# Performance work log

Measured on AMD Instinct MI355X. Metric: run time of the kernel, lower is better.

## Reference

```python
import jax, jax.numpy as jnp
import numpy as np

PENALTY_LAMBDA = 0.5
MAX_RULES = 512
INIT_GATE_LOGIT = -2.0


def setup_inputs() -> dict:
    key = jax.random.key(0)
    k1, k2, k3 = jax.random.split(key, 3)
    B, V, E = 64, 128000, 1000000
    logits = jax.random.normal(k1, (B, V), dtype=jnp.float32)
    # learned per-rule gate logits (nn.Parameter initialized at init_gate_logit;
    # we perturb slightly so gradients are non-degenerate)
    gate_logits = jnp.full((MAX_RULES,), INIT_GATE_LOGIT, dtype=jnp.float32) \
        + 0.1 * jax.random.normal(k2, (MAX_RULES,), dtype=jnp.float32)
    # flattened ragged (rule, token) violation pairs
    kr, kt = jax.random.split(k3)
    rule_ids = jax.random.randint(kr, (E,), 0, MAX_RULES, dtype=jnp.int32)
    token_ids = jax.random.randint(kt, (E,), 0, V, dtype=jnp.int32)
    return {"logits": logits, "gate_logits": gate_logits,
            "rule_ids": rule_ids, "token_ids": token_ids}


def reference(logits, gate_logits, rule_ids, token_ids):
    # eval-mode binary concrete gate (no noise, no thresholding): sigmoid(logit)
    gates = jax.nn.sigmoid(gate_logits)                      # [R]
    V = logits.shape[-1]
    # gated penalty value per (rule, token) pair, single vectorized scatter-add
    vals = gates[rule_ids] * jnp.asarray(PENALTY_LAMBDA, logits.dtype)  # [E]
    pen_1d = jnp.zeros((V,), dtype=logits.dtype).at[token_ids].add(vals)  # [V]
    penalties = jnp.broadcast_to(pen_1d[None, :], logits.shape)           # [B,V]
    modified = logits - penalties
    # coverage loss: -mean of gates over rules that fire (have >=1 violation)
    firing = jnp.zeros((MAX_RULES,), dtype=logits.dtype).at[rule_ids].set(1.0)
    n_firing = jnp.maximum(firing.sum(), 1.0)
    coverage_loss = -(gates * firing).sum() / n_firing
    return modified, coverage_loss, penalties
```

## Files before the change

kernel.cpp:

```cpp
#include <hip/hip_runtime.h>

#define PENALTY_LAMBDA 0.5f
#define RULES 512
#define NR 4
#define RS 32000
#define VOCAB 128000
#define G 64
#define NB 64
#define CH 500
#define CJ 125

typedef float    f32x4 __attribute__((ext_vector_type(4)));
typedef _Float16 f16x4 __attribute__((ext_vector_type(4)));


__global__ void __launch_bounds__(1024) scatter_kernel(
    const int* __restrict__ rule_ids, const int* __restrict__ token_ids,
    const float* __restrict__ gate_logits, _Float16* __restrict__ partials,
    unsigned* __restrict__ masks, int E) {
    __shared__ __align__(16) float hist[RS];
    __shared__ float s_g[RULES];
    __shared__ unsigned char s_f[RULES];
    int t = threadIdx.x;
    int g = blockIdx.x;
    int r = blockIdx.y;
    for (int i = t * 4; i < RS; i += 1024 * 4)
        *(f32x4*)(hist + i) = (f32x4){0.f, 0.f, 0.f, 0.f};
    if (t < RULES) {
        float x = gate_logits[t];
        s_g[t] = PENALTY_LAMBDA / (1.0f + expf(-x));
    }
    if (t >= 512 && t < 512 + RULES / 4) ((unsigned*)s_f)[t - 512] = 0u;
    __syncthreads();

    const int lo = r * RS;
    const int stride = G * 1024 * 4;
    for (int base = (g * 1024 + t) * 4; base + 4 <= E; base += stride) {
        int4 tt = *(const int4*)(token_ids + base);
        int4 rr = *(const int4*)(rule_ids + base);
        int ts[4] = {tt.x, tt.y, tt.z, tt.w};
        int rv[4] = {rr.x, rr.y, rr.z, rr.w};
#pragma unroll
        for (int k = 0; k < 4; ++k) {
            int tok = ts[k] - lo;
            if ((unsigned)tok < (unsigned)RS) atomicAdd(&hist[tok], s_g[rv[k]]);
            if (r == 0) s_f[rv[k]] = 1;
        }
    }
    if (g == 0 && t == 0) {
        for (int e = E & ~3; e < E; ++e) {
            int tok = token_ids[e] - lo; int ru = rule_ids[e];
            if ((unsigned)tok < (unsigned)RS) atomicAdd(&hist[tok], s_g[ru]);
            if (r == 0) s_f[ru] = 1;
        }
    }
    __syncthreads();

    _Float16* dst = partials + ((size_t)r * G + g) * RS;
    for (int i = t * 4; i < RS; i += 1024 * 4) {
        f32x4 s = *(const f32x4*)(&hist[i]);
        f16x4 h = {(_Float16)s.x, (_Float16)s.y, (_Float16)s.z, (_Float16)s.w};
        *(f16x4*)(dst + i) = h;
    }

    if (r == 0 && t < 16) {
        const unsigned* w = (const unsigned*)s_f + t * 8;
        unsigned m = 0;
#pragma unroll
        for (int k = 0; k < 8; ++k) {
            unsigned d = w[k];
            if (d & 0x000000FFu) m |= 1u << (k * 4 + 0);
            if (d & 0x0000FF00u) m |= 1u << (k * 4 + 1);
            if (d & 0x00FF0000u) m |= 1u << (k * 4 + 2);
            if (d & 0xFF000000u) m |= 1u << (k * 4 + 3);
        }
        masks[g * 16 + t] = m;
    }
}

__global__ void __launch_bounds__(512) fused_kernel(
    const _Float16* __restrict__ partials, const unsigned* __restrict__ masks,
    const float* __restrict__ gate_logits, const float* __restrict__ logits,
    float* __restrict__ out_mod, float* __restrict__ out_pen,
    float* __restrict__ out_loss) {
    __shared__ float s_pc[CH + 4];
    __shared__ f32x4 s_part[4][CJ + 1];
    int t = threadIdx.x;
    int tx = t & 127, ty = t >> 7;
    int chunk = blockIdx.x;
    int c0 = chunk * CH;
    int r = c0 / RS;
    int bin = c0 - r * RS;

    {
        if (tx < CJ) {
            f32x4 acc = {0.f, 0.f, 0.f, 0.f};
            const _Float16* bp = partials + ((size_t)r * G + ty * 16) * RS
                               + bin + tx * 4;
#pragma unroll 4
            for (int g = 0; g < 16; ++g) {
                f16x4 h = *(const f16x4*)(bp + (size_t)g * RS);
                acc += (f32x4){(float)h.x, (float)h.y, (float)h.z, (float)h.w};
            }
            s_part[ty][tx] = acc;
        } else if (tx == 127) {
            f32x4 e = {0.f, 0.f, 0.f, 0.f};
            for (int i = 0; i < 4; ++i) {
                int gb = c0 + CH + i; if (gb >= VOCAB) gb -= VOCAB;
                int r2 = gb / RS, b2 = gb - r2 * RS;
                const _Float16* bp2 = partials + ((size_t)r2 * G + ty * 16) * RS + b2;
                float s = 0.f;
                for (int g = 0; g < 16; ++g) s += (float)bp2[(size_t)g * RS];
                ((float*)&e)[i] = s;
            }
            s_part[ty][CJ] = e;
        }
    }
    __syncthreads();
    if (t < CJ + 1) {
        f32x4 s = s_part[0][t] + s_part[1][t] + s_part[2][t] + s_part[3][t];
        *(f32x4*)(s_pc + t * 4) = s;
    }
    __syncthreads();

    if (chunk == 0) {
        __shared__ unsigned s_mask[16];
        __shared__ float sg[8], sf[8];
        if (t < 16) {
            unsigned m = 0;
            for (int g = 0; g < G; ++g) m |= masks[g * 16 + t];
            s_mask[t] = m;
        }
        __syncthreads();
        float f = ((s_mask[t >> 5] >> (t & 31)) & 1u) ? 1.f : 0.f;
        float gf = f / (1.f + expf(-gate_logits[t]));
        for (int off = 32; off > 0; off >>= 1) {
            gf += __shfl_down(gf, off, 64);
            f  += __shfl_down(f,  off, 64);
        }
        if ((t & 63) == 0) { sg[t >> 6] = gf; sf[t >> 6] = f; }
        __syncthreads();
        if (t == 0) {
            float tg = 0.f, tf = 0.f;
            for (int w = 0; w < 8; ++w) { tg += sg[w]; tf += sf[w]; }
            *out_loss = -tg / fmaxf(tf, 1.0f);
            out_pen[0] = s_pc[0];
            out_pen[1] = s_pc[1];
            out_pen[2] = s_pc[2];
        }
    }

    if (tx >= CJ) return;
    f32x4 p0 = *(const f32x4*)(s_pc + tx * 4);
    f32x4 ps = {s_pc[tx * 4 + 3], s_pc[tx * 4 + 4],
                s_pc[tx * 4 + 5], s_pc[tx * 4 + 6]};
    bool glast = (chunk == 255 && tx == CJ - 1);
    size_t col = (size_t)c0 + tx * 4;
#pragma unroll 4
    for (int ib = 0; ib < NB / 4; ++ib) {
        int b = ib * 4 + ty;
        size_t base = (size_t)b * VOCAB + col;
        f32x4 l = __builtin_nontemporal_load((const f32x4*)(logits + base));
        __builtin_nontemporal_store(l - p0, (f32x4*)(out_mod + base));
        if (glast && b == NB - 1) {
            out_pen[base + 3] = p0.w;
        } else {
            __builtin_nontemporal_store(ps, (f32x4*)(out_pen + base + 3));
        }
    }
}

extern "C" void kernel_launch(void* const* d_in, const int* in_sizes, int n_in,
                              void* d_out, int out_size, void* d_ws, size_t ws_size,
                              hipStream_t stream) {
    const float* logits      = (const float*)d_in[0];
    const float* gate_logits = (const float*)d_in[1];
    const int*   rule_ids    = (const int*)d_in[2];
    const int*   token_ids   = (const int*)d_in[3];
    float* out = (float*)d_out;

    const int E = in_sizes[2];
    const size_t BV = (size_t)NB * VOCAB;

    _Float16* partials = (_Float16*)d_ws;
    unsigned* masks    = (unsigned*)(partials + (size_t)NR * G * RS);

    scatter_kernel<<<dim3(G, NR), 1024, 0, stream>>>(
        rule_ids, token_ids, gate_logits, partials, masks, E);

    fused_kernel<<<VOCAB / CH, 512, 0, stream>>>(
        partials, masks, gate_logits, logits,
        out, out + BV + 1, out + BV);
}
```

Before: 122.3 us.

## Pre-partition violation pairs by vocab range before shared-memory scatter

Adds a partition kernel that uses wave ballots to bucket packed (token, rule) pairs into four vocab ranges. Each scatter block then reads only the pairs for its range instead of every block scanning all E pairs and discarding three quarters of them. The cost is an extra kernel launch and a write and re-read of the bucketed pairs. It also switches to unsafeAtomicAdd and replaces the nontemporal loads and stores in the fused kernel with plain ones.

```diff
diff --git a/kernel.cpp b/kernel.cpp
--- a/kernel.cpp
+++ b/kernel.cpp
@@ -9,61 +9,50 @@
 #define NB 64
 #define CH 500
 #define CJ 125
+#define PB 512
+#define PT 256
+#define PW (PB * PT / 64)
 
 typedef float    f32x4 __attribute__((ext_vector_type(4)));
 typedef _Float16 f16x4 __attribute__((ext_vector_type(4)));
 
 
-__global__ void __launch_bounds__(1024) scatter_kernel(
+__global__ void __launch_bounds__(PT) part_kernel(
     const int* __restrict__ rule_ids, const int* __restrict__ token_ids,
-    const float* __restrict__ gate_logits, _Float16* __restrict__ partials,
-    unsigned* __restrict__ masks, int E) {
-    __shared__ __align__(16) float hist[RS];
-    __shared__ float s_g[RULES];
+    unsigned* __restrict__ bucket, unsigned* __restrict__ cnts,
+    unsigned* __restrict__ masks, int E, int iters, int wcap) {
     __shared__ unsigned char s_f[RULES];
-    int t = threadIdx.x;
-    int g = blockIdx.x;
-    int r = blockIdx.y;
-    for (int i = t * 4; i < RS; i += 1024 * 4)
-        *(f32x4*)(hist + i) = (f32x4){0.f, 0.f, 0.f, 0.f};
-    if (t < RULES) {
-        float x = gate_logits[t];
-        s_g[t] = PENALTY_LAMBDA / (1.0f + expf(-x));
-    }
-    if (t >= 512 && t < 512 + RULES / 4) ((unsigned*)s_f)[t - 512] = 0u;
-    __syncthreads();
-
-    const int lo = r * RS;
-    const int stride = G * 1024 * 4;
-    for (int base = (g * 1024 + t) * 4; base + 4 <= E; base += stride) {
-        int4 tt = *(const int4*)(token_ids + base);
-        int4 rr = *(const int4*)(rule_ids + base);
-        int ts[4] = {tt.x, tt.y, tt.z, tt.w};
-        int rv[4] = {rr.x, rr.y, rr.z, rr.w};
-#pragma unroll
-        for (int k = 0; k < 4; ++k) {
-            int tok = ts[k] - lo;
-            if ((unsigned)tok < (unsigned)RS) atomicAdd(&hist[tok], s_g[rv[k]]);
-            if (r == 0) s_f[rv[k]] = 1;
-        }
-    }
-    if (g == 0 && t == 0) {
-        for (int e = E & ~3; e < E; ++e) {
-            int tok = token_ids[e] - lo; int ru = rule_ids[e];
-            if ((unsigned)tok < (unsigned)RS) atomicAdd(&hist[tok], s_g[ru]);
-            if (r == 0) s_f[ru] = 1;
-        }
-    }
-    __syncthreads();
-
-    _Float16* dst = partials + ((size_t)r * G + g) * RS;
-    for (int i = t * 4; i < RS; i += 1024 * 4) {
-        f32x4 s = *(const f32x4*)(&hist[i]);
-        f16x4 h = {(_Float16)s.x, (_Float16)s.y, (_Float16)s.z, (_Float16)s.w};
-        *(f16x4*)(dst + i) = h;
-    }
-
-    if (r == 0 && t < 16) {
+    int t = threadIdx.x, bid = blockIdx.x;
+    if (t < RULES / 4) ((unsigned*)s_f)[t] = 0u;
+    __syncthreads();
+    int lane = t & 63;
+    int wid = bid * (PT / 64) + (t >> 6);
+    unsigned long long ltm = (1ULL << lane) - 1ULL;
+    unsigned cap = (unsigned)PW * (unsigned)wcap;
+    unsigned wbase = (unsigned)wid * (unsigned)wcap;
+    unsigned w0 = 0, w1 = 0, w2 = 0, w3 = 0;
+
+    for (int it = 0; it < iters; ++it) {
+        int i = bid * PT + t + it * (PB * PT);
+        bool v = i < E;
+        int tok = 0, ru = 0;
+        if (v) { tok = token_ids[i]; ru = rule_ids[i]; s_f[ru] = 1; }
+        int r = (unsigned)tok / RS;
+        unsigned p = (unsigned)(tok - r * RS) | ((unsigned)ru << 15);
+#define PART_RANGE(RR, W)                                                  \
+        { unsigned long long m = __ballot(v && r == RR);                   \
+          if (m) { int pos = __popcll(m & ltm);                            \
+                   if (v && r == RR) bucket[RR * cap + wbase + W + pos] = p;\
+                   W += (unsigned)__popcll(m); } }
+        PART_RANGE(0, w0) PART_RANGE(1, w1) PART_RANGE(2, w2) PART_RANGE(3, w3)
+#undef PART_RANGE
+    }
+    if (lane == 0) {
+        unsigned* c = cnts + wid * 4;
+        c[0] = w0; c[1] = w1; c[2] = w2; c[3] = w3;
+    }
+    __syncthreads();
+    if (t < 16) {
         const unsigned* w = (const unsigned*)s_f + t * 8;
         unsigned m = 0;
 #pragma unroll
@@ -74,7 +63,43 @@
             if (d & 0x00FF0000u) m |= 1u << (k * 4 + 2);
             if (d & 0xFF000000u) m |= 1u << (k * 4 + 3);
         }
-        masks[g * 16 + t] = m;
+        masks[bid * 16 + t] = m;
+    }
+}
+
+__global__ void __launch_bounds__(1024) scatter_kernel(
+    const unsigned* __restrict__ bucket, const unsigned* __restrict__ cnts,
+    const float* __restrict__ gate_logits, _Float16* __restrict__ partials,
+    int wcap) {
+    __shared__ __align__(16) float hist[RS];
+    __shared__ float s_g[RULES];
+    int t = threadIdx.x;
+    int g = blockIdx.x;
+    int r = blockIdx.y;
+    for (int i = t * 4; i < RS; i += 1024 * 4)
+        *(f32x4*)(hist + i) = (f32x4){0.f, 0.f, 0.f, 0.f};
+    if (t < RULES)
+        s_g[t] = PENALTY_LAMBDA / (1.0f + expf(-gate_logits[t]));
+    __syncthreads();
+
+    unsigned cap = (unsigned)PW * (unsigned)wcap;
+    const int WPB = PW / G;
+    for (int w = 0; w < WPB; ++w) {
+        int wid = g * WPB + w;
+        unsigned cnt = cnts[wid * 4 + r];
+        const unsigned* bp = bucket + r * cap + (unsigned)wid * (unsigned)wcap;
+        for (unsigned i = t; i < cnt; i += 1024) {
+            unsigned p = bp[i];
+            unsafeAtomicAdd(&hist[p & 32767u], s_g[p >> 15]);
+        }
+    }
+    __syncthreads();
+
+    _Float16* dst = partials + ((size_t)r * G + g) * RS;
+    for (int i = t * 4; i < RS; i += 1024 * 4) {
+        f32x4 s = *(const f32x4*)(&hist[i]);
+        f16x4 h = {(_Float16)s.x, (_Float16)s.y, (_Float16)s.z, (_Float16)s.w};
+        *(f16x4*)(dst + i) = h;
     }
 }
 
@@ -128,7 +153,7 @@
         __shared__ float sg[8], sf[8];
         if (t < 16) {
             unsigned m = 0;
-            for (int g = 0; g < G; ++g) m |= masks[g * 16 + t];
+            for (int g = 0; g < PB; ++g) m |= masks[g * 16 + t];
             s_mask[t] = m;
         }
         __syncthreads();
@@ -160,12 +185,12 @@
     for (int ib = 0; ib < NB / 4; ++ib) {
         int b = ib * 4 + ty;
         size_t base = (size_t)b * VOCAB + col;
-        f32x4 l = __builtin_nontemporal_load((const f32x4*)(logits + base));
-        __builtin_nontemporal_store(l - p0, (f32x4*)(out_mod + base));
+        f32x4 l = *(const f32x4*)(logits + base);
+        *(f32x4*)(out_mod + base) = l - p0;
         if (glast && b == NB - 1) {
             out_pen[base + 3] = p0.w;
         } else {
-            __builtin_nontemporal_store(ps, (f32x4*)(out_pen + base + 3));
+            *(f32x4*)(out_pen + base + 3) = ps;
         }
     }
 }
@@ -182,11 +207,19 @@
     const int E = in_sizes[2];
     const size_t BV = (size_t)NB * VOCAB;
 
-    _Float16* partials = (_Float16*)d_ws;
-    unsigned* masks    = (unsigned*)(partials + (size_t)NR * G * RS);
+    int iters = (E + PB * PT - 1) / (PB * PT);
+    int wcap  = iters * 64;
+
+    unsigned* bucket   = (unsigned*)d_ws;
+    unsigned* cnts     = bucket + (size_t)4 * PW * wcap;
+    unsigned* masks    = cnts + (size_t)PW * 4;
+    _Float16* partials = (_Float16*)(masks + (size_t)PB * 16);
+
+    part_kernel<<<PB, PT, 0, stream>>>(
+        rule_ids, token_ids, bucket, cnts, masks, E, iters, wcap);
 
     scatter_kernel<<<dim3(G, NR), 1024, 0, stream>>>(
-        rule_ids, token_ids, gate_logits, partials, masks, E);
+        bucket, cnts, gate_logits, partials, wcap);
 
     fused_kernel<<<VOCAB / CH, 512, 0, stream>>>(
         partials, masks, gate_logits, logits,
```

Result: slower. 137.9 us (+12.8%).
